# Performance work log

Measured on AMD Instinct MI355X. Metric: run time of the kernel, lower is better.

The kernel has to match this reference:

```python
import jax, jax.numpy as jnp
import numpy as np

B, T, C, H = 8, 2048, 1024, 128

def setup_inputs() -> dict:
    key = jax.random.key(0)
    k1, k2, k3, k4 = jax.random.split(key, 4)
    s = 1.0 / np.sqrt(C)
    return {
        "x": jax.random.normal(k1, (B, T, C), dtype=jnp.float32),
        "Wq": jax.random.normal(k2, (C, H), dtype=jnp.float32) * s,
        "Wk": jax.random.normal(k3, (C, H), dtype=jnp.float32) * s,
        "Wv": jax.random.normal(k4, (C, H), dtype=jnp.float32) * s,
    }

def reference(x, Wq, Wk, Wv):
    # q,k,v: [B,T,H]
    q = jnp.einsum('btc,ch->bth', x, Wq)
    k = jnp.einsum('btc,ch->bth', x, Wk)
    v = jnp.einsum('btc,ch->bth', x, Wv)
    scale = k.shape[-1] ** -0.5
    wei = jnp.einsum('bqh,bkh->bqk', q, k) * scale  # [B,T,T]
    # NOTE: original forward never applies the tril mask -> full bidirectional softmax
    wei = jax.nn.softmax(wei, axis=-1)
    # dropout p=0 (eval): identity
    out = jnp.einsum('bqk,bkh->bqh', wei, v)  # [B,T,H]
    return out
```

## Files before the change

### kernel.cpp

```cpp
#include <hip/hip_runtime.h>

typedef __attribute__((ext_vector_type(4))) float  f32x4;
typedef __attribute__((ext_vector_type(8))) short  s16x8;
typedef __attribute__((ext_vector_type(4))) unsigned int u32x4;
typedef __attribute__((ext_vector_type(4))) unsigned short u16x4;

#define NB 8
#define NT 2048
#define NC 1024
#define NH 128
#define NM (NB * NT)

__device__ __forceinline__ unsigned short f2bf(float f) {
  union { float f; unsigned u; } v; v.f = f;
  unsigned r = v.u + 0x7FFFu + ((v.u >> 16) & 1u);
  return (unsigned short)(r >> 16);
}
__device__ __forceinline__ unsigned pack2(float a, float b) {
  return (unsigned)f2bf(a) | ((unsigned)f2bf(b) << 16);
}
__device__ __forceinline__ f32x4 mfma16(s16x8 a, s16x8 b, f32x4 c) {
  return __builtin_amdgcn_mfma_f32_16x16x32_bf16(a, b, c, 0, 0, 0);
}

__global__ __launch_bounds__(256) void k_prep_w(
    const float* __restrict__ wq, const float* __restrict__ wk,
    const float* __restrict__ wv, unsigned short* __restrict__ wt3) {
  __shared__ float ts[64][65];
  const int tid = threadIdx.x;
  const int w = blockIdx.x >> 5;
  const int rem = blockIdx.x & 31;
  const int c0 = (rem >> 1) * 64;
  const int h0 = (rem & 1) * 64;
  const float* W = (w == 0) ? wq : (w == 1) ? wk : wv;
  const int hl = tid & 63, ci = tid >> 6;
  #pragma unroll
  for (int i = 0; i < 16; ++i) {
    int cl = i * 4 + ci;
    ts[cl][hl] = W[(size_t)(c0 + cl) * NH + h0 + hl];
  }
  __syncthreads();
  const int cl2 = tid & 63, hi2 = tid >> 6;
  #pragma unroll
  for (int j = 0; j < 16; ++j) {
    int hl2 = j * 4 + hi2;
    float v = ts[cl2][hl2];
    if (w == 0) v *= 0.08838834764831845f;
    wt3[(size_t)w * 131072 + (size_t)(h0 + hl2) * NC + c0 + cl2] = f2bf(v);
  }
}

__global__ __launch_bounds__(256, 3) void k_qkv(
    const float* __restrict__ x, const unsigned short* __restrict__ wt3,
    unsigned short* __restrict__ qo, unsigned short* __restrict__ ko,
    unsigned short* __restrict__ vo) {
  __shared__ u32x4 xs4[16384 / 16];
  char* xs = (char*)xs4;
  const int tid = threadIdx.x;
  const int lane = tid & 63;
  const int w = tid >> 6;
  const int m0 = blockIdx.x * 32;
  const int c15 = lane & 15;
  const int g4 = lane >> 4;

  const int sr = tid >> 3;
  const float* xp = x + (size_t)(m0 + sr) * NC + (tid & 7) * 16;
  const int wb = (sr * 256 + (tid & 7) * 32) ^ ((sr & 7) << 4);

  const int n0 = w * 96;
  const int aswz = (c15 & 7) << 4;

  f32x4 acc[2][6] = {};
  f32x4 xr[4];
  #pragma unroll
  for (int j = 0; j < 4; ++j) xr[j] = *(const f32x4*)(xp + j * 4);
  auto pack_write = [&](int buf) {
    u32x4 gA = { pack2(xr[0].x, xr[0].y), pack2(xr[0].z, xr[0].w),
                 pack2(xr[1].x, xr[1].y), pack2(xr[1].z, xr[1].w) };
    u32x4 gB = { pack2(xr[2].x, xr[2].y), pack2(xr[2].z, xr[2].w),
                 pack2(xr[3].x, xr[3].y), pack2(xr[3].z, xr[3].w) };
    *(u32x4*)(xs + buf * 8192 + wb) = gA;
    *(u32x4*)(xs + buf * 8192 + ((sr * 256 + (tid & 7) * 32 + 16) ^ ((sr & 7) << 4))) = gB;
  };
  pack_write(0);
  __syncthreads();

  for (int kt = 0; kt < 8; ++kt) {
    if (kt < 7) {
      #pragma unroll
      for (int j = 0; j < 4; ++j) xr[j] = *(const f32x4*)(xp + (kt + 1) * 128 + j * 4);
    }
    char* cb = xs + (kt & 1) * 8192;
    #pragma unroll
    for (int ks = 0; ks < 4; ++ks) {
      s16x8 a0 = *(const s16x8*)(cb + (((c15)      * 256 + ks * 64 + g4 * 16) ^ aswz));
      s16x8 a1 = *(const s16x8*)(cb + (((c15 + 16) * 256 + ks * 64 + g4 * 16) ^ aswz));
      const unsigned short* wp = wt3 + (size_t)(n0 + c15) * NC
                                 + kt * 128 + ks * 32 + g4 * 8;
      #pragma unroll
      for (int nj = 0; nj < 6; ++nj) {
        s16x8 bf = *(const s16x8*)(wp + (size_t)nj * 16 * NC);
        acc[0][nj] = mfma16(a0, bf, acc[0][nj]);
        acc[1][nj] = mfma16(a1, bf, acc[1][nj]);
      }
    }
    if (kt < 7) pack_write((kt + 1) & 1);
    __syncthreads();
  }
  const int rl = g4 * 4;
  #pragma unroll
  for (int m = 0; m < 2; ++m) {
    #pragma unroll
    for (int nj = 0; nj < 6; ++nj) {
      f32x4 a = acc[m][nj];
      int gcol = n0 + nj * 16 + c15;
      int gr = m0 + m * 16 + rl;
      int h = gcol & 127;
      if (gcol < 256) {
        unsigned short* dst = (gcol < 128) ? qo : ko;
        dst[(size_t)(gr + 0) * NH + h] = f2bf(a.x);
        dst[(size_t)(gr + 1) * NH + h] = f2bf(a.y);
        dst[(size_t)(gr + 2) * NH + h] = f2bf(a.z);
        dst[(size_t)(gr + 3) * NH + h] = f2bf(a.w);
      } else {
        int bb = gr >> 11, tt = gr & 2047;
        u16x4 pv = { f2bf(a.x), f2bf(a.y), f2bf(a.z), f2bf(a.w) };
        *(u16x4*)(vo + ((size_t)(bb * NH + h) * NT + tt)) = pv;
      }
    }
  }
}

__global__ __launch_bounds__(512, 2) void k_attn(
    const unsigned short* __restrict__ qg, const unsigned short* __restrict__ kg,
    const unsigned short* __restrict__ vg, float* __restrict__ out) {
  __shared__ u32x4 lds4[147456 / 16];
  char* L = (char*)lds4;
  const int tid = threadIdx.x;
  const int lane = tid & 63;
  const int w = tid >> 6;
  const int grp = w & 1;
  const int qs = w >> 1;
  const int gl = qs * 64 + lane;
  const int b = blockIdx.y;
  const int qr0 = blockIdx.x * 64;
  const int c15 = lane & 15;
  const int g4 = lane >> 4;
  const int kv0 = grp * 1024;

  char* Kg = L + grp * 65536;
  char* Vg = Kg + 32768;
  char* pw = L + 131072 + w * 2048;

  s16x8 qf[4];
  #pragma unroll
  for (int ks = 0; ks < 4; ++ks)
    qf[ks] = *(const s16x8*)(qg + (size_t)(b * NT + qr0 + qs * 16 + c15) * NH + ks * 32 + g4 * 8);

  float m_run[4], lsum[4];
  #pragma unroll
  for (int r = 0; r < 4; ++r) { m_run[r] = -3.0e38f; lsum[r] = 0.0f; }
  f32x4 acc_o[8] = {};

  const int srow = gl >> 4;
  const unsigned short* kptr = kg + (size_t)(b * NT + kv0 + srow) * NH + (gl & 15) * 8;
  const unsigned short* vptr = vg + (size_t)(b * NH + srow) * NT + kv0 + (gl & 15) * 8;

  u32x4 kreg[8], vreg[8];
  auto stage = [&](int kt) {
    #pragma unroll
    for (int i = 0; i < 8; ++i) {
      kreg[i] = *(const u32x4*)(kptr + ((size_t)(kt * 128 + i * 16)) * NH);
      vreg[i] = *(const u32x4*)(vptr + (size_t)(i * 16) * NT + kt * 128);
    }
  };
  auto write_tiles = [&]() {
    #pragma unroll
    for (int i = 0; i < 8; ++i) {
      int r = srow + i * 16;
      int off = (r * 256 + (gl & 15) * 16) ^ ((r & 7) << 4);
      *(u32x4*)(Kg + off) = kreg[i];
      *(u32x4*)(Vg + off) = vreg[i];
    }
  };
  stage(0);
  write_tiles();
  __syncthreads();

  for (int kt = 0; kt < 8; ++kt) {
    if (kt < 7) stage(kt + 1);
    f32x4 s[8];
    __builtin_amdgcn_s_setprio(1);
    #pragma unroll
    for (int nj = 0; nj < 8; ++nj) {
      f32x4 acc_s = {};
      int kr = nj * 16 + c15;
      int kswz = (kr & 7) << 4;
      #pragma unroll
      for (int ks = 0; ks < 4; ++ks) {
        s16x8 bf = *(const s16x8*)(Kg + ((kr * 256 + ks * 64 + g4 * 16) ^ kswz));
        acc_s = mfma16(qf[ks], bf, acc_s);
      }
      s[nj] = acc_s;
    }
    __builtin_amdgcn_s_setprio(0);
    float alpha[4];
    #pragma unroll
    for (int r = 0; r < 4; ++r) {
      float pm = fmaxf(fmaxf(fmaxf(s[0][r], s[1][r]), fmaxf(s[2][r], s[3][r])),
                       fmaxf(fmaxf(s[4][r], s[5][r]), fmaxf(s[6][r], s[7][r])));
      pm = fmaxf(pm, __shfl_xor(pm, 1));
      pm = fmaxf(pm, __shfl_xor(pm, 2));
      pm = fmaxf(pm, __shfl_xor(pm, 4));
      pm = fmaxf(pm, __shfl_xor(pm, 8));
      float mn = fmaxf(m_run[r], pm);
      alpha[r] = __expf(m_run[r] - mn);
      m_run[r] = mn;
      float psum = 0.0f;
      #pragma unroll
      for (int nj = 0; nj < 8; ++nj) {
        float e = __expf(s[nj][r] - mn);
        s[nj][r] = e;
        psum += e;
      }
      lsum[r] = lsum[r] * alpha[r] + psum;
    }
    #pragma unroll
    for (int hj = 0; hj < 8; ++hj) {
      acc_o[hj][0] *= alpha[0]; acc_o[hj][1] *= alpha[1];
      acc_o[hj][2] *= alpha[2]; acc_o[hj][3] *= alpha[3];
    }
    #pragma unroll
    for (int half = 0; half < 2; ++half) {
      #pragma unroll
      for (int nj = 0; nj < 4; ++nj) {
        #pragma unroll
        for (int r = 0; r < 4; ++r) {
          int row = g4 * 4 + r;
          *(unsigned short*)(pw + ((row * 128 + (nj * 16 + c15) * 2) ^ ((row & 7) << 4)))
              = f2bf(s[half * 4 + nj][r]);
        }
      }
      __builtin_amdgcn_s_setprio(1);
      #pragma unroll
      for (int ks2 = 0; ks2 < 2; ++ks2) {
        s16x8 pa = *(const s16x8*)(pw + ((c15 * 128 + ks2 * 64 + g4 * 16) ^ ((c15 & 7) << 4)));
        int vcb = (half * 2 + ks2) * 64 + g4 * 16;
        #pragma unroll
        for (int hj = 0; hj < 8; ++hj) {
          int vr = hj * 16 + c15;
          s16x8 bv = *(const s16x8*)(Vg + ((vr * 256 + vcb) ^ ((vr & 7) << 4)));
          acc_o[hj] = mfma16(pa, bv, acc_o[hj]);
        }
      }
      __builtin_amdgcn_s_setprio(0);
    }
    __syncthreads();
    if (kt < 7) write_tiles();
    __syncthreads();
  }
  float l_run[4];
  #pragma unroll
  for (int r = 0; r < 4; ++r) {
    float ls = lsum[r];
    ls += __shfl_xor(ls, 1);
    ls += __shfl_xor(ls, 2);
    ls += __shfl_xor(ls, 4);
    ls += __shfl_xor(ls, 8);
    l_run[r] = ls;
  }
  float* msh = (float*)(L + 131072);
  float* lsh = msh + 64;
  if (grp == 1) {
    #pragma unroll
    for (int r = 0; r < 4; ++r) {
      int row = qs * 16 + g4 * 4 + r;
      #pragma unroll
      for (int hj = 0; hj < 8; ++hj)
        *(float*)(L + row * 512 + (hj * 16 + c15) * 4) = acc_o[hj][r];
      if (c15 == 0) { msh[row] = m_run[r]; lsh[row] = l_run[r]; }
    }
  }
  __syncthreads();
  if (grp == 0) {
    #pragma unroll
    for (int r = 0; r < 4; ++r) {
      int row = qs * 16 + g4 * 4 + r;
      float m1 = msh[row], l1 = lsh[row];
      float M = fmaxf(m_run[r], m1);
      float w0 = __expf(m_run[r] - M);
      float w1 = __expf(m1 - M);
      float den = 1.0f / (w0 * l_run[r] + w1 * l1);
      #pragma unroll
      for (int hj = 0; hj < 8; ++hj) {
        float o1 = *(const float*)(L + row * 512 + (hj * 16 + c15) * 4);
        out[(size_t)(b * NT + qr0 + row) * NH + hj * 16 + c15] =
            (w0 * acc_o[hj][r] + w1 * o1) * den;
      }
    }
  }
}

extern "C" void kernel_launch(void* const* d_in, const int* in_sizes, int n_in,
                              void* d_out, int out_size, void* d_ws, size_t ws_size,
                              hipStream_t stream) {
  const float* x  = (const float*)d_in[0];
  const float* wq = (const float*)d_in[1];
  const float* wk = (const float*)d_in[2];
  const float* wv = (const float*)d_in[3];
  unsigned short* ws  = (unsigned short*)d_ws;
  unsigned short* qb  = ws;
  unsigned short* kb  = ws + (size_t)2 * 1024 * 1024;
  unsigned short* vb  = ws + (size_t)4 * 1024 * 1024;
  unsigned short* wt3 = ws + (size_t)6 * 1024 * 1024;

  k_prep_w<<<dim3(96), dim3(256), 0, stream>>>(wq, wk, wv, wt3);
  k_qkv<<<dim3(NM / 32), dim3(256), 0, stream>>>(x, wt3, qb, kb, vb);
  k_attn<<<dim3(NT / 64, NB), dim3(512), 0, stream>>>(qb, kb, vb, (float*)d_out);
}
```

Measured before the change: 191.6 us.

## Retile QKV projection GEMM to 128x192 blocks with 2D warp grid

```diff
diff --git a/kernel.cpp b/kernel.cpp
--- a/kernel.cpp
+++ b/kernel.cpp
@@ -50,27 +50,28 @@
   }
 }
 
-__global__ __launch_bounds__(256, 3) void k_qkv(
+__global__ __launch_bounds__(512, 2) void k_qkv(
     const float* __restrict__ x, const unsigned short* __restrict__ wt3,
     unsigned short* __restrict__ qo, unsigned short* __restrict__ ko,
     unsigned short* __restrict__ vo) {
-  __shared__ u32x4 xs4[16384 / 16];
+  __shared__ u32x4 xs4[32768 / 16];
   char* xs = (char*)xs4;
   const int tid = threadIdx.x;
   const int lane = tid & 63;
   const int w = tid >> 6;
-  const int m0 = blockIdx.x * 32;
+  const int mg = w >> 2;
+  const int ng = w & 3;
+  const int m0 = blockIdx.x * 128;
+  const int n0 = blockIdx.y * 192 + ng * 48;
   const int c15 = lane & 15;
   const int g4 = lane >> 4;
 
-  const int sr = tid >> 3;
-  const float* xp = x + (size_t)(m0 + sr) * NC + (tid & 7) * 16;
-  const int wb = (sr * 256 + (tid & 7) * 32) ^ ((sr & 7) << 4);
-
-  const int n0 = w * 96;
-  const int aswz = (c15 & 7) << 4;
-
-  f32x4 acc[2][6] = {};
+  const int sr = tid >> 2;
+  const float* xp = x + (size_t)(m0 + sr) * NC + (tid & 3) * 16;
+  const int wbA = (sr * 128 + (tid & 3) * 32) ^ ((sr & 7) << 4);
+  const int wbB = (sr * 128 + (tid & 3) * 32 + 16) ^ ((sr & 7) << 4);
+
+  f32x4 acc[4][3] = {};
   f32x4 xr[4];
   #pragma unroll
   for (int j = 0; j < 4; ++j) xr[j] = *(const f32x4*)(xp + j * 4);
@@ -79,42 +80,49 @@
                  pack2(xr[1].x, xr[1].y), pack2(xr[1].z, xr[1].w) };
     u32x4 gB = { pack2(xr[2].x, xr[2].y), pack2(xr[2].z, xr[2].w),
                  pack2(xr[3].x, xr[3].y), pack2(xr[3].z, xr[3].w) };
-    *(u32x4*)(xs + buf * 8192 + wb) = gA;
-    *(u32x4*)(xs + buf * 8192 + ((sr * 256 + (tid & 7) * 32 + 16) ^ ((sr & 7) << 4))) = gB;
+    *(u32x4*)(xs + buf * 16384 + wbA) = gA;
+    *(u32x4*)(xs + buf * 16384 + wbB) = gB;
   };
   pack_write(0);
   __syncthreads();
 
-  for (int kt = 0; kt < 8; ++kt) {
-    if (kt < 7) {
-      #pragma unroll
-      for (int j = 0; j < 4; ++j) xr[j] = *(const f32x4*)(xp + (kt + 1) * 128 + j * 4);
-    }
-    char* cb = xs + (kt & 1) * 8192;
-    #pragma unroll
-    for (int ks = 0; ks < 4; ++ks) {
-      s16x8 a0 = *(const s16x8*)(cb + (((c15)      * 256 + ks * 64 + g4 * 16) ^ aswz));
-      s16x8 a1 = *(const s16x8*)(cb + (((c15 + 16) * 256 + ks * 64 + g4 * 16) ^ aswz));
-      const unsigned short* wp = wt3 + (size_t)(n0 + c15) * NC
-                                 + kt * 128 + ks * 32 + g4 * 8;
-      #pragma unroll
-      for (int nj = 0; nj < 6; ++nj) {
-        s16x8 bf = *(const s16x8*)(wp + (size_t)nj * 16 * NC);
-        acc[0][nj] = mfma16(a0, bf, acc[0][nj]);
-        acc[1][nj] = mfma16(a1, bf, acc[1][nj]);
-      }
-    }
-    if (kt < 7) pack_write((kt + 1) & 1);
+  const int aswz = (c15 & 7) << 4;
+  for (int kt = 0; kt < 16; ++kt) {
+    if (kt < 15) {
+      #pragma unroll
+      for (int j = 0; j < 4; ++j) xr[j] = *(const f32x4*)(xp + (kt + 1) * 64 + j * 4);
+    }
+    s16x8 wf[2][3];
+    {
+      const unsigned short* wpb = wt3 + (size_t)(n0 + c15) * NC + kt * 64 + g4 * 8;
+      #pragma unroll
+      for (int ks = 0; ks < 2; ++ks)
+        #pragma unroll
+        for (int nj = 0; nj < 3; ++nj)
+          wf[ks][nj] = *(const s16x8*)(wpb + (size_t)nj * 16 * NC + ks * 32);
+    }
+    char* cb = xs + (kt & 1) * 16384;
+    #pragma unroll
+    for (int ks = 0; ks < 2; ++ks) {
+      #pragma unroll
+      for (int mf = 0; mf < 4; ++mf) {
+        int arow = mg * 64 + mf * 16 + c15;
+        s16x8 af = *(const s16x8*)(cb + ((arow * 128 + ks * 64 + g4 * 16) ^ aswz));
+        #pragma unroll
+        for (int nj = 0; nj < 3; ++nj)
+          acc[mf][nj] = mfma16(af, wf[ks][nj], acc[mf][nj]);
+      }
+    }
+    if (kt < 15) pack_write((kt + 1) & 1);
     __syncthreads();
   }
-  const int rl = g4 * 4;
-  #pragma unroll
-  for (int m = 0; m < 2; ++m) {
-    #pragma unroll
-    for (int nj = 0; nj < 6; ++nj) {
-      f32x4 a = acc[m][nj];
+  #pragma unroll
+  for (int mf = 0; mf < 4; ++mf) {
+    #pragma unroll
+    for (int nj = 0; nj < 3; ++nj) {
+      f32x4 a = acc[mf][nj];
       int gcol = n0 + nj * 16 + c15;
-      int gr = m0 + m * 16 + rl;
+      int gr = m0 + mg * 64 + mf * 16 + g4 * 4;
       int h = gcol & 127;
       if (gcol < 256) {
         unsigned short* dst = (gcol < 128) ? qo : ko;
@@ -315,6 +323,6 @@
   unsigned short* wt3 = ws + (size_t)6 * 1024 * 1024;
 
   k_prep_w<<<dim3(96), dim3(256), 0, stream>>>(wq, wk, wv, wt3);
-  k_qkv<<<dim3(NM / 32), dim3(256), 0, stream>>>(x, wt3, qb, kb, vb);
+  k_qkv<<<dim3(128, 2), dim3(512), 0, stream>>>(x, wt3, qb, kb, vb);
   k_attn<<<dim3(NT / 64, NB), dim3(512), 0, stream>>>(qb, kb, vb, (float*)d_out);
 }
```

New measurement: 184.0 us. 1.04x faster.
